# Performance work log

Measured on AMD Instinct MI355X. Metric: run time of the kernel, lower is better.

Reference implementation:

```python
import jax, jax.numpy as jnp
import numpy as np

N = 50000      # nodes
E = 800000     # edges (avg degree 16)
G = 128        # g_dim (input feature dim)
H1 = 128       # h1_dim (RGCN output dim)
H2 = 32        # h2_dim (per-head channels)
HEADS = 4
R = 6          # num_relations
OUT = H2 * HEADS  # 128, BatchNorm width
BN_EPS = 1e-5


def setup_inputs() -> dict:
    key = jax.random.key(0)
    k = jax.random.split(key, 16)
    s = 0.05
    return {
        "node_features": jax.random.normal(k[0], (N, G), jnp.float32),
        "node_type": jax.random.randint(k[1], (N,), 0, 3),
        "edge_index": jax.random.randint(k[2], (2, E), 0, N),
        "edge_type": jax.random.randint(k[3], (E,), 0, R),
        # RGCNConv params (root_weight=True, bias=True, aggr='mean')
        "W_rel": jax.random.normal(k[4], (R, G, H1), jnp.float32) * s,
        "W_root": jax.random.normal(k[5], (G, H1), jnp.float32) * s,
        "b_rgcn": jnp.zeros((H1,), jnp.float32),
        # TransformerConv params (concat=True, root_weight=True via lin_skip)
        "Wq": jax.random.normal(k[6], (H1, OUT), jnp.float32) * s,
        "bq": jnp.zeros((OUT,), jnp.float32),
        "Wk": jax.random.normal(k[7], (H1, OUT), jnp.float32) * s,
        "bk": jnp.zeros((OUT,), jnp.float32),
        "Wv": jax.random.normal(k[8], (H1, OUT), jnp.float32) * s,
        "bv": jnp.zeros((OUT,), jnp.float32),
        "Wskip": jax.random.normal(k[9], (H1, OUT), jnp.float32) * s,
        "bskip": jnp.zeros((OUT,), jnp.float32),
        # BatchNorm1d affine params
        "bn_gamma": jnp.ones((OUT,), jnp.float32),
        "bn_beta": jnp.zeros((OUT,), jnp.float32),
    }


def _gnn_forward(node_features, edge_index, edge_type,
                 W_rel, W_root, b_rgcn,
                 Wq, bq, Wk, bk, Wv, bv, Wskip, bskip,
                 bn_gamma, bn_beta):
    src, dst = edge_index[0], edge_index[1]  # message flows src (j) -> dst (i)

    # ---- RGCNConv with mean aggregation per relation ----
    # Transform all nodes under every relation: [R, N, H1]
    xt = jnp.einsum('nd,rdo->rno', node_features, W_rel)
    msg = xt[edge_type, src]                          # [E, H1]
    seg = edge_type * N + dst                         # composite (relation, dst) segment id
    agg = jax.ops.segment_sum(msg, seg, num_segments=R * N).reshape(R, N, H1)
    cnt = jax.ops.segment_sum(jnp.ones((E,), msg.dtype), seg,
                              num_segments=R * N).reshape(R, N)
    x = node_features @ W_root + b_rgcn + (agg / jnp.maximum(cnt, 1.0)[:, :, None]).sum(0)

    # ---- TransformerConv (heads=HEADS, concat=True) ----
    q = (x @ Wq + bq).reshape(N, HEADS, H2)
    kk = (x @ Wk + bk).reshape(N, HEADS, H2)
    v = (x @ Wv + bv).reshape(N, HEADS, H2)

    score = (q[dst] * kk[src]).sum(-1) / np.sqrt(H2)  # [E, HEADS]
    m = jax.ops.segment_max(score, dst, num_segments=N)   # -inf for isolated nodes
    m = jnp.where(jnp.isfinite(m), m, 0.0)
    ex = jnp.exp(score - m[dst])
    den = jax.ops.segment_sum(ex, dst, num_segments=N)
    alpha = ex / (den[dst] + 1e-16)                   # [E, HEADS]

    out = jax.ops.segment_sum(alpha[:, :, None] * v[src], dst,
                              num_segments=N).reshape(N, OUT)
    out = out + x @ Wskip + bskip                     # skip / root connection

    # ---- BatchNorm1d (training-mode batch stats) + LeakyReLU(0.01) ----
    mu = out.mean(0)
    var = out.var(0)  # biased, as torch uses for normalization
    y = (out - mu) * jax.lax.rsqrt(var + BN_EPS) * bn_gamma + bn_beta
    return jax.nn.leaky_relu(y, negative_slope=0.01)


def reference(node_features, node_type, edge_index, edge_type,
              W_rel, W_root, b_rgcn,
              Wq, bq, Wk, bk, Wv, bv, Wskip, bskip,
              bn_gamma, bn_beta):
    # node_type is accepted but unused, matching the original forward.
    return _gnn_forward(node_features, edge_index, edge_type,
                        W_rel, W_root, b_rgcn,
                        Wq, bq, Wk, bk, Wv, bv, Wskip, bskip,
                        bn_gamma, bn_beta)
```

## Files before the change

### kernel.cpp

```cpp
#include <hip/hip_runtime.h>
#include <hip/hip_fp16.h>
#include <stdint.h>

#define G      128
#define OUTW   128
#define RNUM   6

typedef unsigned short us;
typedef _Float16 f16x8 __attribute__((ext_vector_type(8)));
typedef float    f32x4 __attribute__((ext_vector_type(4)));

__device__ inline float h2f(us u) { __half h; *(us*)&h = u; return __half2float(h); }
__device__ inline us f2h(float f) { __half h = __float2half(f); return *(us*)&h; }

union FragU { f16x8 v; ushort4 u[2]; };

__global__ void count_kernel(const int* __restrict__ ei, const int* __restrict__ et,
                             int* __restrict__ segcnt, int N, int E) {
    int e = blockIdx.x * blockDim.x + threadIdx.x;
    if (e >= E) return;
    int dst = ei[E + e];
    int r   = et[e];
    atomicAdd(&segcnt[dst * RNUM + r], 1);
}

__global__ __launch_bounds__(256)
void scan_part(const int* __restrict__ cnt, int* __restrict__ bsum, int n) {
    __shared__ int s[256];
    int base = blockIdx.x * 1024, t = threadIdx.x;
    int v = 0;
    for (int j = 0; j < 4; ++j) { int idx = base + j * 256 + t; if (idx < n) v += cnt[idx]; }
    s[t] = v; __syncthreads();
    for (int off = 128; off; off >>= 1) { if (t < off) s[t] += s[t + off]; __syncthreads(); }
    if (!t) bsum[blockIdx.x] = s[0];
}

__global__ __launch_bounds__(512)
void scan_top(const int* __restrict__ bsum, int* __restrict__ boff,
              int* __restrict__ segptr, int nb, int n) {
    __shared__ int s[512];
    int t = threadIdx.x;
    int v = (t < nb) ? bsum[t] : 0;
    s[t] = v;
    __syncthreads();
    for (int off = 1; off < 512; off <<= 1) {
        int y = (t >= off) ? s[t - off] : 0;
        __syncthreads();
        s[t] += y;
        __syncthreads();
    }
    if (t < nb) boff[t + 1] = s[t];
    if (!t) boff[0] = 0;
    if (t == nb - 1) segptr[n] = s[t];
}

__global__ __launch_bounds__(256)
void scan_apply(const int* __restrict__ cnt, const int* __restrict__ boff,
                int* __restrict__ segptr, int* __restrict__ cursor, int n) {
    __shared__ int L[1024];
    __shared__ int SS[256];
    int base = blockIdx.x * 1024, t = threadIdx.x;
    for (int j = 0; j < 4; ++j) { int idx = base + j * 256 + t; L[j * 256 + t] = (idx < n) ? cnt[idx] : 0; }
    __syncthreads();
    int s0 = L[t*4] + L[t*4+1] + L[t*4+2] + L[t*4+3];
    SS[t] = s0; __syncthreads();
    for (int off = 1; off < 256; off <<= 1) {
        int y = (t >= off) ? SS[t - off] : 0;
        __syncthreads();
        SS[t] += y;
        __syncthreads();
    }
    int e0 = (t ? SS[t - 1] : 0) + boff[blockIdx.x];
    int4 ov;
    int a;
    a = L[t*4+0]; ov.x = e0; e0 += a;
    a = L[t*4+1]; ov.y = e0; e0 += a;
    a = L[t*4+2]; ov.z = e0; e0 += a;
    a = L[t*4+3]; ov.w = e0; e0 += a;
    int idx0 = base + t * 4;
    if (idx0 + 3 < n) {
        *(int4*)(segptr + idx0) = ov;
        *(int4*)(cursor + idx0) = ov;
    } else {
        int vals[4] = {ov.x, ov.y, ov.z, ov.w};
        for (int k = 0; k < 4; ++k)
            if (idx0 + k < n) { segptr[idx0 + k] = vals[k]; cursor[idx0 + k] = vals[k]; }
    }
}

__global__ void scatter_kernel(const int* __restrict__ ei, const int* __restrict__ et,
                               int* __restrict__ cursor, unsigned* __restrict__ esrc,
                               int N, int E) {
    int e = blockIdx.x * blockDim.x + threadIdx.x;
    if (e >= E) return;
    int src = ei[e];
    int dst = ei[E + e];
    int r   = et[e];
    int pos = atomicAdd(&cursor[dst * RNUM + r], 1);
    esrc[pos] = (unsigned)src;
}

__global__ void xhalf_kernel(const float* __restrict__ x, us* __restrict__ xh, int total8) {
    int i = blockIdx.x * blockDim.x + threadIdx.x;
    if (i >= total8) return;
    float4 a = ((const float4*)x)[2*i];
    float4 b = ((const float4*)x)[2*i+1];
    ushort4 u0 = { f2h(a.x), f2h(a.y), f2h(a.z), f2h(a.w) };
    ushort4 u1 = { f2h(b.x), f2h(b.y), f2h(b.z), f2h(b.w) };
    ((ushort4*)xh)[2*i]   = u0;
    ((ushort4*)xh)[2*i+1] = u1;
}

__global__ __launch_bounds__(256)
void wconv_rgcn(const float* __restrict__ Wrel, const float* __restrict__ Wroot,
                ushort4* __restrict__ Btr) {
    int idx = blockIdx.x * 256 + threadIdx.x;
    if (idx >= 224 * 128) return;
    int kq = idx >> 7, n = idx & 127;
    ushort4 o;
    us* op = (us*)&o;
#pragma unroll
    for (int i = 0; i < 4; ++i) {
        int k = 4 * kq + i;
        float v = (k < 768) ? Wrel[(size_t)k * 128 + n] : Wroot[(size_t)(k - 768) * 128 + n];
        op[i] = f2h(v);
    }
    Btr[idx] = o;
}

__global__ __launch_bounds__(256)
void wconv_qkvs(const float* __restrict__ Wq, const float* __restrict__ Wk,
                const float* __restrict__ Wv, const float* __restrict__ Ws,
                ushort4* __restrict__ Btq) {
    int idx = blockIdx.x * 256 + threadIdx.x;
    if (idx >= 32 * 512) return;
    int kq = idx >> 9, n = idx & 511;
    int quad = n >> 7, nl = n & 127;
    const float* W = (quad == 0) ? Wq : (quad == 1) ? Wk : (quad == 2) ? Wv : Ws;
    ushort4 o;
    us* op = (us*)&o;
#pragma unroll
    for (int i = 0; i < 4; ++i) {
        int k = 4 * kq + i;
        op[i] = f2h(W[(size_t)k * 128 + nl]);
    }
    Btq[idx] = o;
}

__global__ __launch_bounds__(256)
void rgcn_fused(const us* __restrict__ xh, const int* __restrict__ segptr,
                const unsigned* __restrict__ esrc, const ushort4* __restrict__ Btr,
                const float* __restrict__ brg, us* __restrict__ xrh, int N) {
    __shared__ ushort4 Ald[64][33];
    const int tid = threadIdx.x;
    const int w = tid >> 6, l = tid & 63;
    const int lh = l >> 4, lm = l & 15;
    const int base = blockIdx.x * 64;
    const int arow = w * 16 + lm;

    f32x4 acc[8];
#pragma unroll
    for (int ct = 0; ct < 8; ++ct) {
        float b = brg[ct * 16 + lm];
        acc[ct] = (f32x4){b, b, b, b};
    }

    for (int ch = 0; ch < 7; ++ch) {
        __syncthreads();
        for (int j = 0; j < 16; ++j) {
            const int row = w * 16 + j;
            const int i = base + row;
            float2 a = {0.f, 0.f};
            if (i < N) {
                if (ch < 6) {
                    int s0 = __builtin_amdgcn_readfirstlane(segptr[i * RNUM + ch]);
                    int s1 = __builtin_amdgcn_readfirstlane(segptr[i * RNUM + ch + 1]);
                    int e = s0;
                    for (; e + 4 <= s1; e += 4) {
                        unsigned q0 = __builtin_amdgcn_readfirstlane(esrc[e]);
                        unsigned q1 = __builtin_amdgcn_readfirstlane(esrc[e + 1]);
                        unsigned q2 = __builtin_amdgcn_readfirstlane(esrc[e + 2]);
                        unsigned q3 = __builtin_amdgcn_readfirstlane(esrc[e + 3]);
                        ushort2 u0 = *(const ushort2*)(xh + (size_t)q0 * G + 2 * l);
                        ushort2 u1 = *(const ushort2*)(xh + (size_t)q1 * G + 2 * l);
                        ushort2 u2 = *(const ushort2*)(xh + (size_t)q2 * G + 2 * l);
                        ushort2 u3 = *(const ushort2*)(xh + (size_t)q3 * G + 2 * l);
                        a.x += (h2f(u0.x) + h2f(u1.x)) + (h2f(u2.x) + h2f(u3.x));
                        a.y += (h2f(u0.y) + h2f(u1.y)) + (h2f(u2.y) + h2f(u3.y));
                    }
                    for (; e < s1; ++e) {
                        unsigned q0 = __builtin_amdgcn_readfirstlane(esrc[e]);
                        ushort2 u0 = *(const ushort2*)(xh + (size_t)q0 * G + 2 * l);
                        a.x += h2f(u0.x);
                        a.y += h2f(u0.y);
                    }
                    float sc = 1.f / fmaxf((float)(s1 - s0), 1.f);
                    a.x *= sc; a.y *= sc;
                } else {
                    ushort2 u = *(const ushort2*)(xh + (size_t)i * G + 2 * l);
                    a.x = h2f(u.x); a.y = h2f(u.y);
                }
            }
            ushort2 t = { f2h(a.x), f2h(a.y) };
            *((ushort2*)&Ald[row][l >> 1] + (l & 1)) = t;
        }
        __syncthreads();
#pragma unroll
        for (int s = 0; s < 4; ++s) {
            FragU af;
            const int kql = s * 8 + lh;
            af.u[0] = Ald[arow][kql];
            af.u[1] = Ald[arow][kql + 4];
            const int kqg = ch * 32 + kql;
            const ushort4* B0 = Btr + (size_t)kqg * 128;
            const ushort4* B1 = Btr + (size_t)(kqg + 4) * 128;
#pragma unroll
            for (int ct = 0; ct < 8; ++ct) {
                FragU bf;
                bf.u[0] = B0[ct * 16 + lm];
                bf.u[1] = B1[ct * 16 + lm];
                acc[ct] = __builtin_amdgcn_mfma_f32_16x16x32_f16(af.v, bf.v, acc[ct], 0, 0, 0);
            }
        }
    }

#pragma unroll
    for (int ct = 0; ct < 8; ++ct) {
#pragma unroll
        for (int i = 0; i < 4; ++i) {
            int r = base + w * 16 + 4 * lh + i;
            if (r < N) xrh[(size_t)r * 128 + ct * 16 + lm] = f2h(acc[ct][i]);
        }
    }
}

__global__ __launch_bounds__(256)
void qkvs_mfma(const us* __restrict__ xrh, const ushort4* __restrict__ Btq,
               const float* __restrict__ bq, const float* __restrict__ bk,
               const float* __restrict__ bv, const float* __restrict__ bs,
               float* __restrict__ qs, us* __restrict__ kvh, int N) {
    __shared__ ushort4 Ald[32 * 16];
    const int tid = threadIdx.x;
    const int w = tid >> 6, l = tid & 63;
    const int lh = l >> 4, lm = l & 15;
    const int base = blockIdx.x * 16;

    {
        int row = tid >> 4, k0 = (tid & 15) * 8;
        int gi = base + row;
        int4 d0 = {0,0,0,0};
        if (gi < N) d0 = *(const int4*)(xrh + (size_t)gi * 128 + k0);
        int kqb = k0 >> 2;
        Ald[(kqb + 0) * 16 + row] = ((ushort4*)&d0)[0];
        Ald[(kqb + 1) * 16 + row] = ((ushort4*)&d0)[1];
    }
    __syncthreads();

    const float* bias = (w == 0) ? bq : (w == 1) ? bk : (w == 2) ? bv : bs;
    f32x4 acc[8];
#pragma unroll
    for (int ct = 0; ct < 8; ++ct) {
        float b = bias[ct * 16 + lm];
        acc[ct] = (f32x4){b, b, b, b};
    }

#pragma unroll
    for (int s = 0; s < 4; ++s) {
        FragU af;
        int kq = s * 8 + lh;
        af.u[0] = Ald[kq * 16 + lm];
        af.u[1] = Ald[(kq + 4) * 16 + lm];
        const ushort4* B0 = Btq + (size_t)kq * 512 + w * 128;
        const ushort4* B1 = Btq + (size_t)(kq + 4) * 512 + w * 128;
#pragma unroll
        for (int ct = 0; ct < 8; ++ct) {
            FragU bf;
            bf.u[0] = B0[ct * 16 + lm];
            bf.u[1] = B1[ct * 16 + lm];
            acc[ct] = __builtin_amdgcn_mfma_f32_16x16x32_f16(af.v, bf.v, acc[ct], 0, 0, 0);
        }
    }

    if (w == 0 || w == 3) {
        int off = (w == 0) ? 0 : 128;
#pragma unroll
        for (int ct = 0; ct < 8; ++ct)
#pragma unroll
            for (int i = 0; i < 4; ++i) {
                int r = base + 4 * lh + i;
                if (r < N) qs[(size_t)r * 256 + off + ct * 16 + lm] = acc[ct][i];
            }
    } else {
        int off = (w == 1) ? 0 : 2;
#pragma unroll
        for (int ct = 0; ct < 8; ++ct)
#pragma unroll
            for (int i = 0; i < 4; ++i) {
                int r = base + 4 * lh + i;
                int col = ct * 16 + lm;
                if (r < N) kvh[(size_t)r * 256 + (col >> 1) * 4 + (col & 1) + off] = f2h(acc[ct][i]);
            }
    }
}

__global__ __launch_bounds__(256)
void attn_kernel(const float* __restrict__ qs, const us* __restrict__ kvh,
                 const int* __restrict__ segptr, const unsigned* __restrict__ esrc,
                 float* __restrict__ out, int N) {
    const int wv = threadIdx.x >> 6, l = threadIdx.x & 63;
    const int i = blockIdx.x * 4 + wv;
    if (i >= N) return;
    const float QS = 0.17677669529663687f;

    float2 q2 = *(const float2*)(qs + (size_t)i * 256 + 2*l);
    q2.x *= QS; q2.y *= QS;

    float m = -INFINITY, den = 0.f;
    float2 acc = {0.f, 0.f};
    const int e0 = segptr[(size_t)i * RNUM], e1 = segptr[(size_t)i * RNUM + RNUM];

#define KVLOAD(P) (*(const ushort4*)(kvh + (size_t)(P) * 256 + 4*l))
#define SCORE(U, S) { \
    float s_ = q2.x * h2f((U).x) + q2.y * h2f((U).y); \
    s_ += __shfl_xor(s_, 1, 16); s_ += __shfl_xor(s_, 2, 16); \
    s_ += __shfl_xor(s_, 4, 16); s_ += __shfl_xor(s_, 8, 16); \
    S = s_; }

    for (int base = e0; base < e1; base += 64) {
        const int nc = min(64, e1 - base);
        unsigned pv = 0;
        if (base + l < e1) pv = esrc[base + l];
        int j = 0;
        for (; j + 4 <= nc; j += 4) {
            unsigned p0 = (unsigned)__shfl((int)pv, j+0);
            unsigned p1 = (unsigned)__shfl((int)pv, j+1);
            unsigned p2 = (unsigned)__shfl((int)pv, j+2);
            unsigned p3 = (unsigned)__shfl((int)pv, j+3);
            ushort4 k0 = KVLOAD(p0), k1 = KVLOAD(p1), k2 = KVLOAD(p2), k3 = KVLOAD(p3);
            float s0, s1, s2, s3;
            SCORE(k0, s0); SCORE(k1, s1); SCORE(k2, s2); SCORE(k3, s3);
            float mx = fmaxf(fmaxf(fmaxf(s0, s1), fmaxf(s2, s3)), m);
            float rs = __expf(m - mx);
            float p0e = __expf(s0 - mx), p1e = __expf(s1 - mx);
            float p2e = __expf(s2 - mx), p3e = __expf(s3 - mx);
            den = den * rs + ((p0e + p1e) + (p2e + p3e));
            acc.x = acc.x * rs + p0e*h2f(k0.z) + p1e*h2f(k1.z) + p2e*h2f(k2.z) + p3e*h2f(k3.z);
            acc.y = acc.y * rs + p0e*h2f(k0.w) + p1e*h2f(k1.w) + p2e*h2f(k2.w) + p3e*h2f(k3.w);
            m = mx;
        }
        for (; j < nc; ++j) {
            unsigned p0 = (unsigned)__shfl((int)pv, j);
            ushort4 k0 = KVLOAD(p0);
            float s0; SCORE(k0, s0);
            float mx = fmaxf(m, s0);
            float rs = __expf(m - mx);
            float pe = __expf(s0 - mx);
            den = den * rs + pe;
            acc.x = acc.x * rs + pe * h2f(k0.z);
            acc.y = acc.y * rs + pe * h2f(k0.w);
            m = mx;
        }
    }
#undef SCORE
#undef KVLOAD

    float inv = 1.f / (den + 1e-16f);
    float2 sk = *(const float2*)(qs + (size_t)i * 256 + 128 + 2*l);
    float2 o = { acc.x * inv + sk.x, acc.y * inv + sk.y };
    *(float2*)(out + (size_t)i * OUTW + 2*l) = o;
}

__global__ __launch_bounds__(256)
void bnreduce_kernel(const float* __restrict__ out, float* __restrict__ bnS,
                     float* __restrict__ bnQ, int N) {
    __shared__ float S[256], Q[256];
    const int tid = threadIdx.x;
    const int col = tid & 127, half = tid >> 7;
    float s = 0.f, q = 0.f;
    for (int r = blockIdx.x * 2 + half; r < N; r += gridDim.x * 2) {
        float v = out[(size_t)r * OUTW + col];
        s += v; q += v * v;
    }
    S[tid] = s; Q[tid] = q;
    __syncthreads();
    if (tid < 128) {
        atomicAdd(&bnS[tid], S[tid] + S[tid + 128]);
        atomicAdd(&bnQ[tid], Q[tid] + Q[tid + 128]);
    }
}

__global__ void bnstats_kernel(const float* __restrict__ bnS, const float* __restrict__ bnQ,
                               const float* __restrict__ gamma, const float* __restrict__ beta,
                               float* __restrict__ bnA, float* __restrict__ bnB, int N) {
    int c = threadIdx.x;
    if (c >= 128) return;
    float fN  = (float)N;
    float mu  = bnS[c] / fN;
    float var = bnQ[c] / fN - mu * mu;
    float rv  = rsqrtf(var + 1e-5f);
    float A   = rv * gamma[c];
    bnA[c] = A;
    bnB[c] = beta[c] - mu * A;
}

__global__ void apply_kernel(float* __restrict__ out, const float* __restrict__ bnA,
                             const float* __restrict__ bnB, int total4) {
    int idx4 = blockIdx.x * blockDim.x + threadIdx.x;
    if (idx4 >= total4) return;
    float4 v = ((const float4*)out)[idx4];
    int c0 = (idx4 * 4) & 127;
    float y;
    y = bnA[c0    ] * v.x + bnB[c0    ]; v.x = (y > 0.f) ? y : 0.01f * y;
    y = bnA[c0 + 1] * v.y + bnB[c0 + 1]; v.y = (y > 0.f) ? y : 0.01f * y;
    y = bnA[c0 + 2] * v.z + bnB[c0 + 2]; v.z = (y > 0.f) ? y : 0.01f * y;
    y = bnA[c0 + 3] * v.w + bnB[c0 + 3]; v.w = (y > 0.f) ? y : 0.01f * y;
    ((float4*)out)[idx4] = v;
}

static inline char* alignp(char* p) {
    return (char*)(((uintptr_t)p + 255) & ~(uintptr_t)255);
}

extern "C" void kernel_launch(void* const* d_in, const int* in_sizes, int n_in,
                              void* d_out, int out_size, void* d_ws, size_t ws_size,
                              hipStream_t stream) {
    const float* x     = (const float*)d_in[0];
    const int*   ei    = (const int*)  d_in[2];
    const int*   et    = (const int*)  d_in[3];
    const float* Wrel  = (const float*)d_in[4];
    const float* Wroot = (const float*)d_in[5];
    const float* brg   = (const float*)d_in[6];
    const float* Wq    = (const float*)d_in[7];
    const float* bq    = (const float*)d_in[8];
    const float* Wk    = (const float*)d_in[9];
    const float* bk    = (const float*)d_in[10];
    const float* Wv    = (const float*)d_in[11];
    const float* bv    = (const float*)d_in[12];
    const float* Wsk   = (const float*)d_in[13];
    const float* bsk   = (const float*)d_in[14];
    const float* gamma = (const float*)d_in[15];
    const float* beta  = (const float*)d_in[16];
    float* out = (float*)d_out;

    const int N = in_sizes[0] / G;
    const int E = in_sizes[3];
    const int NSEG = N * RNUM;
    const int NB_SCAN = (NSEG + 1023) / 1024;

    char* w = (char*)d_ws;
    int* segcnt = (int*)w;           w += (size_t)NSEG * 4;
    float* bnS = (float*)w;          w += 128 * 4;
    float* bnQ = (float*)w;          w += 128 * 4;
    float* bnA = (float*)w;          w += 128 * 4;
    float* bnB = (float*)w;          w += 128 * 4;
    size_t zero_bytes = (size_t)(w - (char*)d_ws);
    w = alignp(w);
    int* bsum  = (int*)w;            w += 512 * 4;
    int* boff  = (int*)w;            w += 513 * 4;
    w = alignp(w);
    int* segptr = (int*)w;           w += (size_t)(NSEG + 1) * 4;
    w = alignp(w);
    int* cursor = (int*)w;           w += (size_t)NSEG * 4;
    w = alignp(w);
    unsigned* esrc = (unsigned*)w;   w += (size_t)E * 4;
    w = alignp(w);
    us* xh     = (us*)w;             w += (size_t)N * G * 2;
    w = alignp(w);
    us* xrh    = (us*)w;             w += (size_t)N * OUTW * 2;
    w = alignp(w);
    ushort4* Btr = (ushort4*)w;      w += (size_t)224 * 128 * 8;
    w = alignp(w);
    ushort4* Btq = (ushort4*)w;      w += (size_t)32 * 512 * 8;
    w = alignp(w);
    float* qs  = (float*)w;          w += (size_t)N * 256 * 4;
    w = alignp(w);
    us* kvh    = (us*)w;             w += (size_t)N * 256 * 2;

    hipMemsetAsync(d_ws, 0, zero_bytes, stream);

    int eb = (E + 255) / 256;
    count_kernel<<<eb, 256, 0, stream>>>(ei, et, segcnt, N, E);

    scan_part<<<NB_SCAN, 256, 0, stream>>>(segcnt, bsum, NSEG);
    scan_top<<<1, 512, 0, stream>>>(bsum, boff, segptr, NB_SCAN, NSEG);
    scan_apply<<<NB_SCAN, 256, 0, stream>>>(segcnt, boff, segptr, cursor, NSEG);

    scatter_kernel<<<eb, 256, 0, stream>>>(ei, et, cursor, esrc, N, E);

    int total8 = N * G / 8;
    xhalf_kernel<<<(total8 + 255) / 256, 256, 0, stream>>>(x, xh, total8);

    wconv_rgcn<<<112, 256, 0, stream>>>(Wrel, Wroot, Btr);
    wconv_qkvs<<<64, 256, 0, stream>>>(Wq, Wk, Wv, Wsk, Btq);

    rgcn_fused<<<(N + 63) / 64, 256, 0, stream>>>(xh, segptr, esrc, Btr, brg, xrh, N);

    qkvs_mfma<<<(N + 15) / 16, 256, 0, stream>>>(xrh, Btq, bq, bk, bv, bsk, qs, kvh, N);

    attn_kernel<<<(N + 3) / 4, 256, 0, stream>>>(qs, kvh, segptr, esrc, out, N);

    bnreduce_kernel<<<200, 256, 0, stream>>>(out, bnS, bnQ, N);
    bnstats_kernel<<<1, 128, 0, stream>>>(bnS, bnQ, gamma, beta, bnA, bnB, N);

    int total4 = N * OUTW / 4;
    apply_kernel<<<(total4 + 255) / 256, 256, 0, stream>>>(out, bnA, bnB, total4);
}
```

Before: 525.9 us.

## Split RGCN aggregation from MFMA, fuse prep, BN reduce, and stats kernels

The fused RGCN kernel is split into a per-node wave aggregation kernel and a separate MFMA GEMM. The aggregation kernel walks all six relations in one pass, loads edge source indices with shuffles, and writes per-relation means in an MFMA-ready tiled layout. The three conversion kernels become one prep kernel. BatchNorm sum and sum-of-squares move into a grid-stride attention kernel, and the stats computation moves into the apply kernel. The QKVS GEMM now reads A fragments directly from global memory with 512-thread blocks, and the mean buffer aliases the qs workspace. This adds a write and read of an N×768 half buffer in exchange for more parallel gathers and fewer launches.

Result: faster. 500.8 us (-4.8%).

```diff
diff --git a/kernel.cpp b/kernel.cpp
--- a/kernel.cpp
+++ b/kernel.cpp
@@ -100,63 +100,127 @@
     esrc[pos] = (unsigned)src;
 }
 
-__global__ void xhalf_kernel(const float* __restrict__ x, us* __restrict__ xh, int total8) {
-    int i = blockIdx.x * blockDim.x + threadIdx.x;
-    if (i >= total8) return;
-    float4 a = ((const float4*)x)[2*i];
-    float4 b = ((const float4*)x)[2*i+1];
-    ushort4 u0 = { f2h(a.x), f2h(a.y), f2h(a.z), f2h(a.w) };
-    ushort4 u1 = { f2h(b.x), f2h(b.y), f2h(b.z), f2h(b.w) };
-    ((ushort4*)xh)[2*i]   = u0;
-    ((ushort4*)xh)[2*i+1] = u1;
-}
-
-__global__ __launch_bounds__(256)
-void wconv_rgcn(const float* __restrict__ Wrel, const float* __restrict__ Wroot,
-                ushort4* __restrict__ Btr) {
-    int idx = blockIdx.x * 256 + threadIdx.x;
-    if (idx >= 224 * 128) return;
-    int kq = idx >> 7, n = idx & 127;
-    ushort4 o;
-    us* op = (us*)&o;
-#pragma unroll
-    for (int i = 0; i < 4; ++i) {
-        int k = 4 * kq + i;
-        float v = (k < 768) ? Wrel[(size_t)k * 128 + n] : Wroot[(size_t)(k - 768) * 128 + n];
-        op[i] = f2h(v);
-    }
-    Btr[idx] = o;
-}
-
-__global__ __launch_bounds__(256)
-void wconv_qkvs(const float* __restrict__ Wq, const float* __restrict__ Wk,
-                const float* __restrict__ Wv, const float* __restrict__ Ws,
-                ushort4* __restrict__ Btq) {
-    int idx = blockIdx.x * 256 + threadIdx.x;
-    if (idx >= 32 * 512) return;
-    int kq = idx >> 9, n = idx & 511;
-    int quad = n >> 7, nl = n & 127;
-    const float* W = (quad == 0) ? Wq : (quad == 1) ? Wk : (quad == 2) ? Wv : Ws;
-    ushort4 o;
-    us* op = (us*)&o;
-#pragma unroll
-    for (int i = 0; i < 4; ++i) {
-        int k = 4 * kq + i;
-        op[i] = f2h(W[(size_t)k * 128 + nl]);
-    }
-    Btq[idx] = o;
-}
-
-__global__ __launch_bounds__(256)
-void rgcn_fused(const us* __restrict__ xh, const int* __restrict__ segptr,
-                const unsigned* __restrict__ esrc, const ushort4* __restrict__ Btr,
-                const float* __restrict__ brg, us* __restrict__ xrh, int N) {
-    __shared__ ushort4 Ald[64][33];
+__global__ __launch_bounds__(256)
+void prep_kernel(const float* __restrict__ x, us* __restrict__ xh,
+                 const float* __restrict__ Wrel, const float* __restrict__ Wroot,
+                 ushort4* __restrict__ Btr,
+                 const float* __restrict__ Wq, const float* __restrict__ Wk,
+                 const float* __restrict__ Wv, const float* __restrict__ Ws,
+                 ushort4* __restrict__ Btq, int xblocks) {
+    int b = blockIdx.x;
+    if (b < xblocks) {
+        int i = b * 256 + threadIdx.x;
+        float4 a = ((const float4*)x)[2*i];
+        float4 c = ((const float4*)x)[2*i+1];
+        ushort4 u0 = { f2h(a.x), f2h(a.y), f2h(a.z), f2h(a.w) };
+        ushort4 u1 = { f2h(c.x), f2h(c.y), f2h(c.z), f2h(c.w) };
+        ((ushort4*)xh)[2*i]   = u0;
+        ((ushort4*)xh)[2*i+1] = u1;
+    } else if (b < xblocks + 112) {
+        int idx = (b - xblocks) * 256 + threadIdx.x;
+        int kq = idx >> 7, n = idx & 127;
+        ushort4 o;
+        us* op = (us*)&o;
+#pragma unroll
+        for (int i = 0; i < 4; ++i) {
+            int k = 4 * kq + i;
+            float v = (k < 768) ? Wrel[(size_t)k * 128 + n] : Wroot[(size_t)(k - 768) * 128 + n];
+            op[i] = f2h(v);
+        }
+        Btr[idx] = o;
+    } else {
+        int idx = (b - xblocks - 112) * 256 + threadIdx.x;
+        int kq = idx >> 9, n = idx & 511;
+        int quad = n >> 7, nl = n & 127;
+        const float* W = (quad == 0) ? Wq : (quad == 1) ? Wk : (quad == 2) ? Wv : Ws;
+        ushort4 o;
+        us* op = (us*)&o;
+#pragma unroll
+        for (int i = 0; i < 4; ++i) {
+            int k = 4 * kq + i;
+            op[i] = f2h(W[(size_t)k * 128 + nl]);
+        }
+        Btq[idx] = o;
+    }
+}
+
+__global__ __launch_bounds__(256)
+void agg_kernel(const us* __restrict__ xh, const int* __restrict__ segptr,
+                const unsigned* __restrict__ esrc, us* __restrict__ meanF, int N) {
+    const int wv = threadIdx.x >> 6, l = threadIdx.x & 63;
+    const int i = blockIdx.x * 4 + wv;
+    if (i >= N) return;
+    const int t = i >> 4, row = i & 15;
+    const int e0 = __builtin_amdgcn_readfirstlane(segptr[i * RNUM]);
+    const int e1 = __builtin_amdgcn_readfirstlane(segptr[i * RNUM + RNUM]);
+
+    int rcur = 0;
+    int sstart = e0;
+    int bnext = __builtin_amdgcn_readfirstlane(segptr[i * RNUM + 1]);
+    float2 a = {0.f, 0.f};
+    us* wbase = meanF + (size_t)t * 12288 + row * 4 + (l & 1) * 2;
+    const int kqo = (l >> 1) * 64;
+
+#define FLUSH() { \
+    float sc_ = 1.f / fmaxf((float)(bnext - sstart), 1.f); \
+    ushort2 t2_ = { f2h(a.x * sc_), f2h(a.y * sc_) }; \
+    *(ushort2*)(wbase + rcur * 2048 + kqo) = t2_; \
+    a.x = 0.f; a.y = 0.f; \
+    sstart = bnext; ++rcur; \
+    if (rcur < RNUM) bnext = __builtin_amdgcn_readfirstlane(segptr[i * RNUM + rcur + 1]); }
+
+#define GET(J) ((unsigned)__shfl((int)pv, (J)))
+#define LX(Q)  (*(const ushort2*)(xh + (size_t)(Q) * G + 2 * l))
+#define STEP(U) { while (p >= bnext && rcur < RNUM - 1) FLUSH(); \
+                  a.x += h2f((U).x); a.y += h2f((U).y); ++p; }
+
+    int p = e0;
+    for (int wb = e0; wb < e1; wb += 64) {
+        const int nc = min(64, e1 - wb);
+        unsigned pv = (wb + l < e1) ? esrc[wb + l] : 0u;
+        int j = 0;
+        while (j + 8 <= nc) {
+            unsigned q0 = GET(j+0), q1 = GET(j+1), q2 = GET(j+2), q3 = GET(j+3);
+            unsigned q4 = GET(j+4), q5 = GET(j+5), q6 = GET(j+6), q7 = GET(j+7);
+            ushort2 u0 = LX(q0), u1 = LX(q1), u2 = LX(q2), u3 = LX(q3);
+            ushort2 u4 = LX(q4), u5 = LX(q5), u6 = LX(q6), u7 = LX(q7);
+            STEP(u0); STEP(u1); STEP(u2); STEP(u3);
+            STEP(u4); STEP(u5); STEP(u6); STEP(u7);
+            j += 8;
+        }
+        while (j + 2 <= nc) {
+            unsigned q0 = GET(j), q1 = GET(j+1);
+            ushort2 u0 = LX(q0), u1 = LX(q1);
+            STEP(u0); STEP(u1);
+            j += 2;
+        }
+        if (j < nc) {
+            unsigned q0 = GET(j);
+            ushort2 u0 = LX(q0);
+            STEP(u0);
+            ++j;
+        }
+    }
+    while (rcur < RNUM) FLUSH();
+#undef STEP
+#undef LX
+#undef GET
+#undef FLUSH
+}
+
+__global__ __launch_bounds__(256)
+void rgcn_mfma2(const us* __restrict__ xh, const us* __restrict__ meanF,
+                const ushort4* __restrict__ Btr, const float* __restrict__ brg,
+                us* __restrict__ xrh, int N) {
     const int tid = threadIdx.x;
     const int w = tid >> 6, l = tid & 63;
     const int lh = l >> 4, lm = l & 15;
     const int base = blockIdx.x * 64;
-    const int arow = w * 16 + lm;
+    const int ntile = N >> 4;
+    const int t  = min(blockIdx.x * 4 + w, ntile - 1);
+    const int gr = min(base + w * 16 + lm, N - 1);
+    const us* amean = meanF + (size_t)t * 12288 + lm * 4;
+    const us* aroot = xh + (size_t)gr * 128;
 
     f32x4 acc[8];
 #pragma unroll
@@ -165,62 +229,26 @@
         acc[ct] = (f32x4){b, b, b, b};
     }
 
-    for (int ch = 0; ch < 7; ++ch) {
-        __syncthreads();
-        for (int j = 0; j < 16; ++j) {
-            const int row = w * 16 + j;
-            const int i = base + row;
-            float2 a = {0.f, 0.f};
-            if (i < N) {
-                if (ch < 6) {
-                    int s0 = __builtin_amdgcn_readfirstlane(segptr[i * RNUM + ch]);
-                    int s1 = __builtin_amdgcn_readfirstlane(segptr[i * RNUM + ch + 1]);
-                    int e = s0;
-                    for (; e + 4 <= s1; e += 4) {
-                        unsigned q0 = __builtin_amdgcn_readfirstlane(esrc[e]);
-                        unsigned q1 = __builtin_amdgcn_readfirstlane(esrc[e + 1]);
-                        unsigned q2 = __builtin_amdgcn_readfirstlane(esrc[e + 2]);
-                        unsigned q3 = __builtin_amdgcn_readfirstlane(esrc[e + 3]);
-                        ushort2 u0 = *(const ushort2*)(xh + (size_t)q0 * G + 2 * l);
-                        ushort2 u1 = *(const ushort2*)(xh + (size_t)q1 * G + 2 * l);
-                        ushort2 u2 = *(const ushort2*)(xh + (size_t)q2 * G + 2 * l);
-                        ushort2 u3 = *(const ushort2*)(xh + (size_t)q3 * G + 2 * l);
-                        a.x += (h2f(u0.x) + h2f(u1.x)) + (h2f(u2.x) + h2f(u3.x));
-                        a.y += (h2f(u0.y) + h2f(u1.y)) + (h2f(u2.y) + h2f(u3.y));
-                    }
-                    for (; e < s1; ++e) {
-                        unsigned q0 = __builtin_amdgcn_readfirstlane(esrc[e]);
-                        ushort2 u0 = *(const ushort2*)(xh + (size_t)q0 * G + 2 * l);
-                        a.x += h2f(u0.x);
-                        a.y += h2f(u0.y);
-                    }
-                    float sc = 1.f / fmaxf((float)(s1 - s0), 1.f);
-                    a.x *= sc; a.y *= sc;
-                } else {
-                    ushort2 u = *(const ushort2*)(xh + (size_t)i * G + 2 * l);
-                    a.x = h2f(u.x); a.y = h2f(u.y);
-                }
-            }
-            ushort2 t = { f2h(a.x), f2h(a.y) };
-            *((ushort2*)&Ald[row][l >> 1] + (l & 1)) = t;
-        }
-        __syncthreads();
-#pragma unroll
-        for (int s = 0; s < 4; ++s) {
-            FragU af;
-            const int kql = s * 8 + lh;
-            af.u[0] = Ald[arow][kql];
-            af.u[1] = Ald[arow][kql + 4];
-            const int kqg = ch * 32 + kql;
-            const ushort4* B0 = Btr + (size_t)kqg * 128;
-            const ushort4* B1 = Btr + (size_t)(kqg + 4) * 128;
-#pragma unroll
-            for (int ct = 0; ct < 8; ++ct) {
-                FragU bf;
-                bf.u[0] = B0[ct * 16 + lm];
-                bf.u[1] = B1[ct * 16 + lm];
-                acc[ct] = __builtin_amdgcn_mfma_f32_16x16x32_f16(af.v, bf.v, acc[ct], 0, 0, 0);
-            }
+#pragma unroll
+    for (int s = 0; s < 28; ++s) {
+        const int kqg = s * 8 + lh;
+        FragU af;
+        if (s < 24) {
+            af.u[0] = *(const ushort4*)(amean + kqg * 64);
+            af.u[1] = *(const ushort4*)(amean + (kqg + 4) * 64);
+        } else {
+            const int kql = kqg - 192;
+            af.u[0] = *(const ushort4*)(aroot + kql * 4);
+            af.u[1] = *(const ushort4*)(aroot + kql * 4 + 16);
+        }
+        const ushort4* B0 = Btr + (size_t)kqg * 128 + lm;
+        const ushort4* B1 = B0 + 4 * 128;
+#pragma unroll
+        for (int ct = 0; ct < 8; ++ct) {
+            FragU bf;
+            bf.u[0] = B0[ct * 16];
+            bf.u[1] = B1[ct * 16];
+            acc[ct] = __builtin_amdgcn_mfma_f32_16x16x32_f16(af.v, bf.v, acc[ct], 0, 0, 0);
         }
     }
 
@@ -234,90 +262,90 @@
     }
 }
 
-__global__ __launch_bounds__(256)
-void qkvs_mfma(const us* __restrict__ xrh, const ushort4* __restrict__ Btq,
-               const float* __restrict__ bq, const float* __restrict__ bk,
-               const float* __restrict__ bv, const float* __restrict__ bs,
-               float* __restrict__ qs, us* __restrict__ kvh, int N) {
-    __shared__ ushort4 Ald[32 * 16];
+__global__ __launch_bounds__(512)
+void qkvs_mfma2(const us* __restrict__ xrh, const ushort4* __restrict__ Btq,
+                const float* __restrict__ bq, const float* __restrict__ bk,
+                const float* __restrict__ bv, const float* __restrict__ bs,
+                float* __restrict__ qs, us* __restrict__ kvh, int N) {
     const int tid = threadIdx.x;
     const int w = tid >> 6, l = tid & 63;
+    const int quad = w & 3, tp = w >> 2;
     const int lh = l >> 4, lm = l & 15;
-    const int base = blockIdx.x * 16;
-
-    {
-        int row = tid >> 4, k0 = (tid & 15) * 8;
-        int gi = base + row;
-        int4 d0 = {0,0,0,0};
-        if (gi < N) d0 = *(const int4*)(xrh + (size_t)gi * 128 + k0);
-        int kqb = k0 >> 2;
-        Ald[(kqb + 0) * 16 + row] = ((ushort4*)&d0)[0];
-        Ald[(kqb + 1) * 16 + row] = ((ushort4*)&d0)[1];
-    }
-    __syncthreads();
-
-    const float* bias = (w == 0) ? bq : (w == 1) ? bk : (w == 2) ? bv : bs;
-    f32x4 acc[8];
-#pragma unroll
-    for (int ct = 0; ct < 8; ++ct) {
-        float b = bias[ct * 16 + lm];
-        acc[ct] = (f32x4){b, b, b, b};
-    }
-
-#pragma unroll
-    for (int s = 0; s < 4; ++s) {
-        FragU af;
-        int kq = s * 8 + lh;
-        af.u[0] = Ald[kq * 16 + lm];
-        af.u[1] = Ald[(kq + 4) * 16 + lm];
-        const ushort4* B0 = Btq + (size_t)kq * 512 + w * 128;
-        const ushort4* B1 = Btq + (size_t)(kq + 4) * 512 + w * 128;
+    const int base = blockIdx.x * 64;
+    const float* bias = (quad == 0) ? bq : (quad == 1) ? bk : (quad == 2) ? bv : bs;
+
+#pragma unroll
+    for (int tt = 0; tt < 2; ++tt) {
+        const int tile = tp * 2 + tt;
+        const int ar = min(base + tile * 16 + lm, N - 1);
+        const us* ap = xrh + (size_t)ar * 128;
+        f32x4 acc[8];
 #pragma unroll
         for (int ct = 0; ct < 8; ++ct) {
-            FragU bf;
-            bf.u[0] = B0[ct * 16 + lm];
-            bf.u[1] = B1[ct * 16 + lm];
-            acc[ct] = __builtin_amdgcn_mfma_f32_16x16x32_f16(af.v, bf.v, acc[ct], 0, 0, 0);
-        }
-    }
-
-    if (w == 0 || w == 3) {
-        int off = (w == 0) ? 0 : 128;
-#pragma unroll
-        for (int ct = 0; ct < 8; ++ct)
-#pragma unroll
-            for (int i = 0; i < 4; ++i) {
-                int r = base + 4 * lh + i;
-                if (r < N) qs[(size_t)r * 256 + off + ct * 16 + lm] = acc[ct][i];
+            float b = bias[ct * 16 + lm];
+            acc[ct] = (f32x4){b, b, b, b};
+        }
+#pragma unroll
+        for (int s = 0; s < 4; ++s) {
+            const int kq = s * 8 + lh;
+            FragU af;
+            af.u[0] = *(const ushort4*)(ap + kq * 4);
+            af.u[1] = *(const ushort4*)(ap + kq * 4 + 16);
+            const ushort4* B0 = Btq + (size_t)kq * 512 + quad * 128 + lm;
+            const ushort4* B1 = B0 + 4 * 512;
+#pragma unroll
+            for (int ct = 0; ct < 8; ++ct) {
+                FragU bf;
+                bf.u[0] = B0[ct * 16];
+                bf.u[1] = B1[ct * 16];
+                acc[ct] = __builtin_amdgcn_mfma_f32_16x16x32_f16(af.v, bf.v, acc[ct], 0, 0, 0);
             }
-    } else {
-        int off = (w == 1) ? 0 : 2;
-#pragma unroll
-        for (int ct = 0; ct < 8; ++ct)
-#pragma unroll
-            for (int i = 0; i < 4; ++i) {
-                int r = base + 4 * lh + i;
-                int col = ct * 16 + lm;
-                if (r < N) kvh[(size_t)r * 256 + (col >> 1) * 4 + (col & 1) + off] = f2h(acc[ct][i]);
-            }
+        }
+        if (quad == 0 || quad == 3) {
+            int off = (quad == 0) ? 0 : 128;
+#pragma unroll
+            for (int ct = 0; ct < 8; ++ct)
+#pragma unroll
+                for (int i = 0; i < 4; ++i) {
+                    int r = base + tile * 16 + 4 * lh + i;
+                    if (r < N) qs[(size_t)r * 256 + off + ct * 16 + lm] = acc[ct][i];
+                }
+        } else {
+            int off = (quad == 1) ? 0 : 2;
+#pragma unroll
+            for (int ct = 0; ct < 8; ++ct)
+#pragma unroll
+                for (int i = 0; i < 4; ++i) {
+                    int r = base + tile * 16 + 4 * lh + i;
+                    int col = ct * 16 + lm;
+                    if (r < N) kvh[(size_t)r * 256 + (col >> 1) * 4 + (col & 1) + off] = f2h(acc[ct][i]);
+                }
+        }
     }
 }
 
 __global__ __launch_bounds__(256)
 void attn_kernel(const float* __restrict__ qs, const us* __restrict__ kvh,
                  const int* __restrict__ segptr, const unsigned* __restrict__ esrc,
-                 float* __restrict__ out, int N) {
-    const int wv = threadIdx.x >> 6, l = threadIdx.x & 63;
-    const int i = blockIdx.x * 4 + wv;
-    if (i >= N) return;
+                 float* __restrict__ out, float* __restrict__ bnS,
+                 float* __restrict__ bnQ, int N) {
+    __shared__ float sS[128], sQ[128];
+    const int tid = threadIdx.x;
+    if (tid < 128) { sS[tid] = 0.f; sQ[tid] = 0.f; }
+    __syncthreads();
+
+    const int wv = tid >> 6, l = tid & 63;
+    const int stride = gridDim.x * 4;
     const float QS = 0.17677669529663687f;
-
-    float2 q2 = *(const float2*)(qs + (size_t)i * 256 + 2*l);
-    q2.x *= QS; q2.y *= QS;
-
-    float m = -INFINITY, den = 0.f;
-    float2 acc = {0.f, 0.f};
-    const int e0 = segptr[(size_t)i * RNUM], e1 = segptr[(size_t)i * RNUM + RNUM];
+    float2 bsum = {0.f, 0.f}, bsq = {0.f, 0.f};
+
+    for (int i = blockIdx.x * 4 + wv; i < N; i += stride) {
+        float2 q2 = *(const float2*)(qs + (size_t)i * 256 + 2*l);
+        q2.x *= QS; q2.y *= QS;
+
+        float m = -INFINITY, den = 0.f;
+        float2 acc = {0.f, 0.f};
+        const int e0 = segptr[(size_t)i * RNUM], e1 = segptr[(size_t)i * RNUM + RNUM];
 
 #define KVLOAD(P) (*(const ushort4*)(kvh + (size_t)(P) * 256 + 4*l))
 #define SCORE(U, S) { \
@@ -326,95 +354,89 @@
     s_ += __shfl_xor(s_, 4, 16); s_ += __shfl_xor(s_, 8, 16); \
     S = s_; }
 
-    for (int base = e0; base < e1; base += 64) {
-        const int nc = min(64, e1 - base);
-        unsigned pv = 0;
-        if (base + l < e1) pv = esrc[base + l];
-        int j = 0;
-        for (; j + 4 <= nc; j += 4) {
-            unsigned p0 = (unsigned)__shfl((int)pv, j+0);
-            unsigned p1 = (unsigned)__shfl((int)pv, j+1);
-            unsigned p2 = (unsigned)__shfl((int)pv, j+2);
-            unsigned p3 = (unsigned)__shfl((int)pv, j+3);
-            ushort4 k0 = KVLOAD(p0), k1 = KVLOAD(p1), k2 = KVLOAD(p2), k3 = KVLOAD(p3);
-            float s0, s1, s2, s3;
-            SCORE(k0, s0); SCORE(k1, s1); SCORE(k2, s2); SCORE(k3, s3);
-            float mx = fmaxf(fmaxf(fmaxf(s0, s1), fmaxf(s2, s3)), m);
-            float rs = __expf(m - mx);
-            float p0e = __expf(s0 - mx), p1e = __expf(s1 - mx);
-            float p2e = __expf(s2 - mx), p3e = __expf(s3 - mx);
-            den = den * rs + ((p0e + p1e) + (p2e + p3e));
-            acc.x = acc.x * rs + p0e*h2f(k0.z) + p1e*h2f(k1.z) + p2e*h2f(k2.z) + p3e*h2f(k3.z);
-            acc.y = acc.y * rs + p0e*h2f(k0.w) + p1e*h2f(k1.w) + p2e*h2f(k2.w) + p3e*h2f(k3.w);
-            m = mx;
-        }
-        for (; j < nc; ++j) {
-            unsigned p0 = (unsigned)__shfl((int)pv, j);
-            ushort4 k0 = KVLOAD(p0);
-            float s0; SCORE(k0, s0);
-            float mx = fmaxf(m, s0);
-            float rs = __expf(m - mx);
-            float pe = __expf(s0 - mx);
-            den = den * rs + pe;
-            acc.x = acc.x * rs + pe * h2f(k0.z);
-            acc.y = acc.y * rs + pe * h2f(k0.w);
-            m = mx;
-        }
-    }
+        for (int base = e0; base < e1; base += 64) {
+            const int nc = min(64, e1 - base);
+            unsigned pv = 0;
+            if (base + l < e1) pv = esrc[base + l];
+            int j = 0;
+            for (; j + 4 <= nc; j += 4) {
+                unsigned p0 = (unsigned)__shfl((int)pv, j+0);
+                unsigned p1 = (unsigned)__shfl((int)pv, j+1);
+                unsigned p2 = (unsigned)__shfl((int)pv, j+2);
+                unsigned p3 = (unsigned)__shfl((int)pv, j+3);
+                ushort4 k0 = KVLOAD(p0), k1 = KVLOAD(p1), k2 = KVLOAD(p2), k3 = KVLOAD(p3);
+                float s0, s1, s2, s3;
+                SCORE(k0, s0); SCORE(k1, s1); SCORE(k2, s2); SCORE(k3, s3);
+                float mx = fmaxf(fmaxf(fmaxf(s0, s1), fmaxf(s2, s3)), m);
+                float rs = __expf(m - mx);
+                float p0e = __expf(s0 - mx), p1e = __expf(s1 - mx);
+                float p2e = __expf(s2 - mx), p3e = __expf(s3 - mx);
+                den = den * rs + ((p0e + p1e) + (p2e + p3e));
+                acc.x = acc.x * rs + p0e*h2f(k0.z) + p1e*h2f(k1.z) + p2e*h2f(k2.z) + p3e*h2f(k3.z);
+                acc.y = acc.y * rs + p0e*h2f(k0.w) + p1e*h2f(k1.w) + p2e*h2f(k2.w) + p3e*h2f(k3.w);
+                m = mx;
+            }
+            for (; j < nc; ++j) {
+                unsigned p0 = (unsigned)__shfl((int)pv, j);
+                ushort4 k0 = KVLOAD(p0);
+                float s0; SCORE(k0, s0);
+                float mx = fmaxf(m, s0);
+                float rs = __expf(m - mx);
+                float pe = __expf(s0 - mx);
+                den = den * rs + pe;
+                acc.x = acc.x * rs + pe * h2f(k0.z);
+                acc.y = acc.y * rs + pe * h2f(k0.w);
+                m = mx;
+            }
+        }
 #undef SCORE
 #undef KVLOAD
 
-    float inv = 1.f / (den + 1e-16f);
-    float2 sk = *(const float2*)(qs + (size_t)i * 256 + 128 + 2*l);
-    float2 o = { acc.x * inv + sk.x, acc.y * inv + sk.y };
-    *(float2*)(out + (size_t)i * OUTW + 2*l) = o;
-}
-
-__global__ __launch_bounds__(256)
-void bnreduce_kernel(const float* __restrict__ out, float* __restrict__ bnS,
-                     float* __restrict__ bnQ, int N) {
-    __shared__ float S[256], Q[256];
-    const int tid = threadIdx.x;
-    const int col = tid & 127, half = tid >> 7;
-    float s = 0.f, q = 0.f;
-    for (int r = blockIdx.x * 2 + half; r < N; r += gridDim.x * 2) {
-        float v = out[(size_t)r * OUTW + col];
-        s += v; q += v * v;
-    }
-    S[tid] = s; Q[tid] = q;
+        float inv = 1.f / (den + 1e-16f);
+        float2 sk = *(const float2*)(qs + (size_t)i * 256 + 128 + 2*l);
+        float2 o = { acc.x * inv + sk.x, acc.y * inv + sk.y };
+        *(float2*)(out + (size_t)i * OUTW + 2*l) = o;
+        bsum.x += o.x; bsum.y += o.y;
+        bsq.x  += o.x * o.x; bsq.y += o.y * o.y;
+    }
+
+    atomicAdd(&sS[2*l],     bsum.x);
+    atomicAdd(&sS[2*l + 1], bsum.y);
+    atomicAdd(&sQ[2*l],     bsq.x);
+    atomicAdd(&sQ[2*l + 1], bsq.y);
     __syncthreads();
     if (tid < 128) {
-        atomicAdd(&bnS[tid], S[tid] + S[tid + 128]);
-        atomicAdd(&bnQ[tid], Q[tid] + Q[tid + 128]);
-    }
-}
-
-__global__ void bnstats_kernel(const float* __restrict__ bnS, const float* __restrict__ bnQ,
-                               const float* __restrict__ gamma, const float* __restrict__ beta,
-                               float* __restrict__ bnA, float* __restrict__ bnB, int N) {
-    int c = threadIdx.x;
-    if (c >= 128) return;
-    float fN  = (float)N;
-    float mu  = bnS[c] / fN;
-    float var = bnQ[c] / fN - mu * mu;
-    float rv  = rsqrtf(var + 1e-5f);
-    float A   = rv * gamma[c];
-    bnA[c] = A;
-    bnB[c] = beta[c] - mu * A;
-}
-
-__global__ void apply_kernel(float* __restrict__ out, const float* __restrict__ bnA,
-                             const float* __restrict__ bnB, int total4) {
-    int idx4 = blockIdx.x * blockDim.x + threadIdx.x;
-    if (idx4 >= total4) return;
-    float4 v = ((const float4*)out)[idx4];
-    int c0 = (idx4 * 4) & 127;
-    float y;
-    y = bnA[c0    ] * v.x + bnB[c0    ]; v.x = (y > 0.f) ? y : 0.01f * y;
-    y = bnA[c0 + 1] * v.y + bnB[c0 + 1]; v.y = (y > 0.f) ? y : 0.01f * y;
-    y = bnA[c0 + 2] * v.z + bnB[c0 + 2]; v.z = (y > 0.f) ? y : 0.01f * y;
-    y = bnA[c0 + 3] * v.w + bnB[c0 + 3]; v.w = (y > 0.f) ? y : 0.01f * y;
-    ((float4*)out)[idx4] = v;
+        atomicAdd(&bnS[tid], sS[tid]);
+        atomicAdd(&bnQ[tid], sQ[tid]);
+    }
+}
+
+__global__ __launch_bounds__(256)
+void apply_kernel(float* __restrict__ out, const float* __restrict__ bnS,
+                  const float* __restrict__ bnQ, const float* __restrict__ gamma,
+                  const float* __restrict__ beta, int N, int total4) {
+    __shared__ float A_s[128], B_s[128];
+    const int tid = threadIdx.x;
+    if (tid < 128) {
+        float fN  = (float)N;
+        float mu  = bnS[tid] / fN;
+        float var = bnQ[tid] / fN - mu * mu;
+        float rv  = rsqrtf(var + 1e-5f);
+        float A   = rv * gamma[tid];
+        A_s[tid] = A;
+        B_s[tid] = beta[tid] - mu * A;
+    }
+    __syncthreads();
+    for (int idx4 = blockIdx.x * 256 + tid; idx4 < total4; idx4 += gridDim.x * 256) {
+        float4 v = ((const float4*)out)[idx4];
+        int c0 = (idx4 * 4) & 127;
+        float y;
+        y = A_s[c0    ] * v.x + B_s[c0    ]; v.x = (y > 0.f) ? y : 0.01f * y;
+        y = A_s[c0 + 1] * v.y + B_s[c0 + 1]; v.y = (y > 0.f) ? y : 0.01f * y;
+        y = A_s[c0 + 2] * v.z + B_s[c0 + 2]; v.z = (y > 0.f) ? y : 0.01f * y;
+        y = A_s[c0 + 3] * v.w + B_s[c0 + 3]; v.w = (y > 0.f) ? y : 0.01f * y;
+        ((float4*)out)[idx4] = v;
+    }
 }
 
 static inline char* alignp(char* p) {
@@ -451,8 +473,6 @@
     int* segcnt = (int*)w;           w += (size_t)NSEG * 4;
     float* bnS = (float*)w;          w += 128 * 4;
     float* bnQ = (float*)w;          w += 128 * 4;
-    float* bnA = (float*)w;          w += 128 * 4;
-    float* bnB = (float*)w;          w += 128 * 4;
     size_t zero_bytes = (size_t)(w - (char*)d_ws);
     w = alignp(w);
     int* bsum  = (int*)w;            w += 512 * 4;
@@ -472,9 +492,9 @@
     w = alignp(w);
     ushort4* Btq = (ushort4*)w;      w += (size_t)32 * 512 * 8;
     w = alignp(w);
-    float* qs  = (float*)w;          w += (size_t)N * 256 * 4;
-    w = alignp(w);
-    us* kvh    = (us*)w;             w += (size_t)N * 256 * 2;
+    us*    meanF = (us*)w;
+    float* qs    = (float*)w;
+    us*    kvh   = (us*)(w + (size_t)N * 256 * 4);
 
     hipMemsetAsync(d_ws, 0, zero_bytes, stream);
 
@@ -487,21 +507,18 @@
 
     scatter_kernel<<<eb, 256, 0, stream>>>(ei, et, cursor, esrc, N, E);
 
-    int total8 = N * G / 8;
-    xhalf_kernel<<<(total8 + 255) / 256, 256, 0, stream>>>(x, xh, total8);
-
-    wconv_rgcn<<<112, 256, 0, stream>>>(Wrel, Wroot, Btr);
-    wconv_qkvs<<<64, 256, 0, stream>>>(Wq, Wk, Wv, Wsk, Btq);
-
-    rgcn_fused<<<(N + 63) / 64, 256, 0, stream>>>(xh, segptr, esrc, Btr, brg, xrh, N);
-
-    qkvs_mfma<<<(N + 15) / 16, 256, 0, stream>>>(xrh, Btq, bq, bk, bv, bsk, qs, kvh, N);
-
-    attn_kernel<<<(N + 3) / 4, 256, 0, stream>>>(qs, kvh, segptr, esrc, out, N);
-
-    bnreduce_kernel<<<200, 256, 0, stream>>>(out, bnS, bnQ, N);
-    bnstats_kernel<<<1, 128, 0, stream>>>(bnS, bnQ, gamma, beta, bnA, bnB, N);
+    int xblocks = N * G / 8 / 256;
+    prep_kernel<<<xblocks + 112 + 64, 256, 0, stream>>>(x, xh, Wrel, Wroot, Btr,
+                                                        Wq, Wk, Wv, Wsk, Btq, xblocks);
+
+    agg_kernel<<<(N + 3) / 4, 256, 0, stream>>>(xh, segptr, esrc, meanF, N);
+
+    rgcn_mfma2<<<(N + 63) / 64, 256, 0, stream>>>(xh, meanF, Btr, brg, xrh, N);
+
+    qkvs_mfma2<<<(N + 63) / 64, 512, 0, stream>>>(xrh, Btq, bq, bk, bv, bsk, qs, kvh, N);
+
+    attn_kernel<<<2048, 256, 0, stream>>>(qs, kvh, segptr, esrc, out, bnS, bnQ, N);
 
     int total4 = N * OUTW / 4;
-    apply_kernel<<<(total4 + 255) / 256, 256, 0, stream>>>(out, bnA, bnB, total4);
-}
+    apply_kernel<<<2048, 256, 0, stream>>>(out, bnS, bnQ, gamma, beta, N, total4);
+}
```
